# Optimization experiments

Measured on AMD Instinct MI355X. Metric: run time of the kernel, lower is better.

The kernel has to match this reference:

```python
import jax, jax.numpy as jnp
import numpy as np

N_NODES = 100000
N_EDGES = 1600000
DIM_IN, DIM_H, DIM_OUT = 128, 128, 64


def setup_inputs() -> dict:
    key = jax.random.key(0)
    ks = jax.random.split(key, 8)
    s = 0.05
    return {
        "x": jax.random.normal(ks[0], (N_NODES, DIM_IN), jnp.float32),
        "edge_index": jax.random.randint(ks[1], (2, N_EDGES), 0, N_NODES, jnp.int64),
        "W_l1": jax.random.normal(ks[2], (DIM_IN, DIM_H), jnp.float32) * s,
        "W_r1": jax.random.normal(ks[3], (DIM_IN, DIM_H), jnp.float32) * s,
        "b1": jax.random.normal(ks[4], (DIM_H,), jnp.float32) * s,
        "W_l2": jax.random.normal(ks[5], (DIM_H, DIM_OUT), jnp.float32) * s,
        "W_r2": jax.random.normal(ks[6], (DIM_H, DIM_OUT), jnp.float32) * s,
        "b2": jax.random.normal(ks[7], (DIM_OUT,), jnp.float32) * s,
    }


def _sage_conv(h, src, dst, n_nodes, W_l, W_r, b):
    # mean-aggregate neighbor features: gather x[src], scatter-sum to dst, divide by in-degree
    msg = h[src]                                              # [E, d]
    agg = jax.ops.segment_sum(msg, dst, num_segments=n_nodes)  # [N, d]
    deg = jax.ops.segment_sum(jnp.ones((src.shape[0],), h.dtype), dst, num_segments=n_nodes)
    mean = agg / jnp.maximum(deg, 1.0)[:, None]
    # out = lin_l(mean) + lin_r(x) ; bias lives on lin_l (PyG SAGEConv default)
    return mean @ W_l + h @ W_r + b


def reference(x, edge_index, W_l1, W_r1, b1, W_l2, W_r2, b2):
    src, dst = edge_index[0], edge_index[1]
    n = x.shape[0]
    h = jax.nn.relu(_sage_conv(x, src, dst, n, W_l1, W_r1, b1))
    # dropout(p=0.5) is identity in eval mode
    return _sage_conv(h, src, dst, n, W_l2, W_r2, b2)
```

## Files before the change

kernel.cpp:

```cpp
#include <hip/hip_runtime.h>

#define NN 100000
#define NE 1600000

typedef __attribute__((ext_vector_type(8))) short bf16x8;
typedef __attribute__((ext_vector_type(4))) float f32x4;

__device__ __forceinline__ float bf2f(unsigned short b) {
    union { unsigned int u; float f; } v;
    v.u = ((unsigned int)b) << 16;
    return v.f;
}
__device__ __forceinline__ unsigned short f2bf(float f) {
    union { float f; unsigned int u; } v; v.f = f;
    unsigned int u = v.u;
    return (unsigned short)((u + 0x7FFFu + ((u >> 16) & 1u)) >> 16);
}

__global__ void detect_kernel(const int* __restrict__ e, int* __restrict__ flag) {
    int t = blockIdx.x * blockDim.x + threadIdx.x;
    if (t < 4096 && e[2 * t + 1] != 0) atomicOr(flag, 1);
}

__device__ __forceinline__ int esrc(const int* e, int mode, int i) {
    return mode ? e[i] : e[2 * i];
}
__device__ __forceinline__ int edst(const int* e, int mode, int i) {
    return mode ? e[NE + i] : e[2 * (NE + i)];
}

#define NRANGE 4
#define RSZ 25000
#define NCHUNK 64
#define EPC (NE / NCHUNK)
#define GS 100352

__global__ __launch_bounds__(1024) void histA_kernel(
    const int* __restrict__ e, const int* __restrict__ flag, int* __restrict__ G) {
    __shared__ int lh[RSZ];
    const int bid = blockIdx.x;
    const int r = bid & (NRANGE - 1);
    const int c = bid >> 2;
    const int lo = r * RSZ;
    for (int idx = threadIdx.x; idx < RSZ; idx += 1024) lh[idx] = 0;
    __syncthreads();
    const int mode = *flag;
    const int base = c * EPC;
    for (int i = base + threadIdx.x; i < base + EPC; i += 1024) {
        int dl = edst(e, mode, i) - lo;
        if ((unsigned)dl < (unsigned)RSZ) atomicAdd(&lh[dl], 1);
    }
    __syncthreads();
    for (int idx = threadIdx.x; idx < RSZ; idx += 1024)
        G[(size_t)c * GS + lo + idx] = lh[idx];
}

__global__ __launch_bounds__(1024) void scatterC_kernel(
    const int* __restrict__ e, const int* __restrict__ flag,
    const int* __restrict__ S, const int* __restrict__ G, int* __restrict__ csr) {
    __shared__ int sOff[RSZ];
    const int bid = blockIdx.x;
    const int r = bid & (NRANGE - 1);
    const int c = bid >> 2;
    const int lo = r * RSZ;
    for (int idx = threadIdx.x; idx < RSZ; idx += 1024)
        sOff[idx] = S[lo + idx] + G[(size_t)c * GS + lo + idx];
    __syncthreads();
    const int mode = *flag;
    const int base = c * EPC;
    for (int i = base + threadIdx.x; i < base + EPC; i += 1024) {
        int dl = edst(e, mode, i) - lo;
        if ((unsigned)dl < (unsigned)RSZ) {
            int s = esrc(e, mode, i);
            csr[atomicAdd(&sOff[dl], 1)] = s;
        }
    }
}

#define PREF_B 391
#define CVT_G 6250

__global__ __launch_bounds__(256) void prefix_cvt_kernel(
    int* __restrict__ G, int* __restrict__ S,
    const float* __restrict__ xin, unsigned short* __restrict__ xb) {
    if (blockIdx.x < PREF_B) {
        int d = blockIdx.x * 256 + threadIdx.x;
        if (d >= NN) return;
        int run = 0;
#pragma unroll 8
        for (int c = 0; c < NCHUNK; c++) {
            size_t idx = (size_t)c * GS + d;
            int t = G[idx];
            G[idx] = run;
            run += t;
        }
        S[d] = run;
    } else {
        long long i = ((long long)(blockIdx.x - PREF_B) * 256 + threadIdx.x) * 8;
        float4 a = *(const float4*)(xin + i);
        float4 b = *(const float4*)(xin + i + 4);
        bf16x8 rv;
        rv[0] = (short)f2bf(a.x); rv[1] = (short)f2bf(a.y);
        rv[2] = (short)f2bf(a.z); rv[3] = (short)f2bf(a.w);
        rv[4] = (short)f2bf(b.x); rv[5] = (short)f2bf(b.y);
        rv[6] = (short)f2bf(b.z); rv[7] = (short)f2bf(b.w);
        *(bf16x8*)(xb + i) = rv;
    }
}

#define SCAN_G 392

__global__ __launch_bounds__(256) void blocksum_kernel(const int* __restrict__ S,
                                                       int* __restrict__ part) {
    int i = blockIdx.x * 256 + threadIdx.x;
    int v = (i < NN) ? S[i] : 0;
#pragma unroll
    for (int off = 32; off; off >>= 1) v += __shfl_down(v, off, 64);
    __shared__ int wsum[4];
    if ((threadIdx.x & 63) == 0) wsum[threadIdx.x >> 6] = v;
    __syncthreads();
    if (threadIdx.x == 0)
        part[blockIdx.x] = wsum[0] + wsum[1] + wsum[2] + wsum[3];
}

__global__ __launch_bounds__(512) void partscan_kernel(int* __restrict__ part) {
    __shared__ int lds[512];
    const int t = threadIdx.x;
    int v = (t < SCAN_G) ? part[t] : 0;
    lds[t] = v;
    __syncthreads();
    for (int off = 1; off < 512; off <<= 1) {
        int u = (t >= off) ? lds[t - off] : 0;
        __syncthreads();
        lds[t] += u;
        __syncthreads();
    }
    if (t < SCAN_G) part[t] = lds[t] - v;
}

__global__ __launch_bounds__(256) void scanfin_kernel(int* __restrict__ S,
                                                      const int* __restrict__ part) {
    __shared__ int lds[256];
    const int t = threadIdx.x;
    const int i = blockIdx.x * 256 + t;
    int v = (i < NN) ? S[i] : 0;
    lds[t] = v;
    __syncthreads();
    for (int off = 1; off < 256; off <<= 1) {
        int u = (t >= off) ? lds[t - off] : 0;
        __syncthreads();
        lds[t] += u;
        __syncthreads();
    }
    if (i < NN) S[i] = lds[t] - v + part[blockIdx.x];
}

template <int D>
__global__ __launch_bounds__(256) void gather_mean_bf16(
    const unsigned short* __restrict__ feat, const int* __restrict__ csr,
    const int* __restrict__ S, unsigned short* __restrict__ out) {
    constexpr int TPN = D / 8;
    constexpr int NPB = 256 / TPN;
    const int tid = threadIdx.x;
    const int node = blockIdx.x * NPB + tid / TPN;
    const int c = tid % TPN;
    if (node >= NN) return;
    const int begin = S[node];
    const int end = (node == NN - 1) ? NE : S[node + 1];
    float acc0[8] = {0.f, 0.f, 0.f, 0.f, 0.f, 0.f, 0.f, 0.f};
    float acc1[8] = {0.f, 0.f, 0.f, 0.f, 0.f, 0.f, 0.f, 0.f};
    int j = begin;
    for (; j + 8 <= end; j += 8) {
        int s0 = csr[j], s1 = csr[j + 1], s2 = csr[j + 2], s3 = csr[j + 3];
        int s4 = csr[j + 4], s5 = csr[j + 5], s6 = csr[j + 6], s7 = csr[j + 7];
        bf16x8 v0 = *(const bf16x8*)(feat + (size_t)s0 * D + 8 * c);
        bf16x8 v1 = *(const bf16x8*)(feat + (size_t)s1 * D + 8 * c);
        bf16x8 v2 = *(const bf16x8*)(feat + (size_t)s2 * D + 8 * c);
        bf16x8 v3 = *(const bf16x8*)(feat + (size_t)s3 * D + 8 * c);
        bf16x8 v4 = *(const bf16x8*)(feat + (size_t)s4 * D + 8 * c);
        bf16x8 v5 = *(const bf16x8*)(feat + (size_t)s5 * D + 8 * c);
        bf16x8 v6 = *(const bf16x8*)(feat + (size_t)s6 * D + 8 * c);
        bf16x8 v7 = *(const bf16x8*)(feat + (size_t)s7 * D + 8 * c);
#pragma unroll
        for (int q = 0; q < 8; q++) {
            acc0[q] += (bf2f((unsigned short)v0[q]) + bf2f((unsigned short)v2[q])) +
                       (bf2f((unsigned short)v4[q]) + bf2f((unsigned short)v6[q]));
            acc1[q] += (bf2f((unsigned short)v1[q]) + bf2f((unsigned short)v3[q])) +
                       (bf2f((unsigned short)v5[q]) + bf2f((unsigned short)v7[q]));
        }
    }
    for (; j + 2 <= end; j += 2) {
        int s0 = csr[j], s1 = csr[j + 1];
        bf16x8 v0 = *(const bf16x8*)(feat + (size_t)s0 * D + 8 * c);
        bf16x8 v1 = *(const bf16x8*)(feat + (size_t)s1 * D + 8 * c);
#pragma unroll
        for (int q = 0; q < 8; q++) {
            acc0[q] += bf2f((unsigned short)v0[q]);
            acc1[q] += bf2f((unsigned short)v1[q]);
        }
    }
    if (j < end) {
        int s = csr[j];
        bf16x8 v = *(const bf16x8*)(feat + (size_t)s * D + 8 * c);
#pragma unroll
        for (int q = 0; q < 8; q++) acc0[q] += bf2f((unsigned short)v[q]);
    }
    const float inv = 1.0f / fmaxf((float)(end - begin), 1.0f);
    bf16x8 r;
#pragma unroll
    for (int q = 0; q < 8; q++) r[q] = (short)f2bf((acc0[q] + acc1[q]) * inv);
    *(bf16x8*)(out + (size_t)node * D + 8 * c) = r;
}

template <int NO, bool DUAL, bool EADD, bool RELU, bool BIAS, bool OUTF32>
__global__ __launch_bounds__(256, 2) void mfma_gemm(
    const unsigned short* __restrict__ A,
    const unsigned short* __restrict__ X,
    const float* __restrict__ Wa,
    const float* __restrict__ Wb,
    const float* __restrict__ bias,
    const unsigned short* __restrict__ E,
    void* __restrict__ Yv, int N) {
    constexpr int NT = NO / 16;
    constexpr int PITCH = 136;
    __shared__ unsigned short sWb[NO * PITCH];
    __shared__ unsigned short sWa[DUAL ? NO * PITCH : 8];

    const int tid = threadIdx.x;
    for (int idx = tid; idx < 128 * NO; idx += 256) {
        int k = idx / NO, n = idx % NO;
        sWb[n * PITCH + k] = f2bf(Wb[idx]);
        if constexpr (DUAL) sWa[n * PITCH + k] = f2bf(Wa[idx]);
    }
    __syncthreads();

    const int lane = tid & 63;
    const int wv = tid >> 6;
    const int r16 = lane & 15;
    const int kg = lane >> 4;
    const long long rowbase = (long long)blockIdx.x * 128 + wv * 32;

    bf16x8 xf[2][4], af[2][4];
    const bf16x8 zz = {0, 0, 0, 0, 0, 0, 0, 0};
#pragma unroll
    for (int rt = 0; rt < 2; rt++) {
        long long row = rowbase + rt * 16 + r16;
        bool ok = row < N;
#pragma unroll
        for (int ks = 0; ks < 4; ks++) {
            xf[rt][ks] = ok ? *(const bf16x8*)(X + row * 128 + ks * 32 + kg * 8) : zz;
            if constexpr (DUAL)
                af[rt][ks] = ok ? *(const bf16x8*)(A + row * 128 + ks * 32 + kg * 8) : zz;
        }
    }

    f32x4 acc[2][NT];
#pragma unroll
    for (int t = 0; t < NT; t++) {
        float bv = 0.f;
        if constexpr (BIAS) bv = bias[t * 16 + r16];
#pragma unroll
        for (int rt = 0; rt < 2; rt++) acc[rt][t] = (f32x4){bv, bv, bv, bv};
    }

#pragma unroll
    for (int t = 0; t < NT; t++) {
        const unsigned short* wp = &sWb[(t * 16 + r16) * PITCH + kg * 8];
        bf16x8 bb[4];
#pragma unroll
        for (int ks = 0; ks < 4; ks++) bb[ks] = *(const bf16x8*)(wp + ks * 32);
        bf16x8 ba[4];
        if constexpr (DUAL) {
            const unsigned short* wq = &sWa[(t * 16 + r16) * PITCH + kg * 8];
#pragma unroll
            for (int ks = 0; ks < 4; ks++) ba[ks] = *(const bf16x8*)(wq + ks * 32);
        }
#pragma unroll
        for (int rt = 0; rt < 2; rt++) {
#pragma unroll
            for (int ks = 0; ks < 4; ks++) {
                acc[rt][t] = __builtin_amdgcn_mfma_f32_16x16x32_bf16(
                    xf[rt][ks], bb[ks], acc[rt][t], 0, 0, 0);
                if constexpr (DUAL)
                    acc[rt][t] = __builtin_amdgcn_mfma_f32_16x16x32_bf16(
                        af[rt][ks], ba[ks], acc[rt][t], 0, 0, 0);
            }
        }
    }

#pragma unroll
    for (int rt = 0; rt < 2; rt++) {
#pragma unroll
        for (int r = 0; r < 4; r++) {
            long long row = rowbase + rt * 16 + kg * 4 + r;
            if (row < N) {
#pragma unroll
                for (int t = 0; t < NT; t++) {
                    int col = t * 16 + r16;
                    float v = acc[rt][t][r];
                    if constexpr (EADD) v += bf2f(E[row * NO + col]);
                    if constexpr (RELU) v = fmaxf(v, 0.f);
                    if constexpr (OUTF32) ((float*)Yv)[row * NO + col] = v;
                    else ((unsigned short*)Yv)[row * NO + col] = f2bf(v);
                }
            }
        }
    }
}

extern "C" void kernel_launch(void* const* d_in, const int* in_sizes, int n_in,
                              void* d_out, int out_size, void* d_ws, size_t ws_size,
                              hipStream_t stream) {
    const float* x    = (const float*)d_in[0];
    const int*   e32  = (const int*)d_in[1];
    const float* W_l1 = (const float*)d_in[2];
    const float* W_r1 = (const float*)d_in[3];
    const float* b1   = (const float*)d_in[4];
    const float* W_l2 = (const float*)d_in[5];
    const float* W_r2 = (const float*)d_in[6];
    const float* b2   = (const float*)d_in[7];
    float* out = (float*)d_out;

    int* wsI = (int*)d_ws;
    int* flag = wsI;
    int* S    = wsI + 1024;
    int* part = wsI + 1024 + 100352;
    int* csr  = wsI + 101888;
    unsigned short* xb = (unsigned short*)(wsI + 1701888);
    int* G = wsI + 8101888;
    unsigned short* mean1b = (unsigned short*)(wsI + 8101888);
    unsigned short* hb     = (unsigned short*)(wsI + 14524416);
    unsigned short* t2b    = xb;
    unsigned short* mean2b = xb + (size_t)NN * 64;

    hipMemsetAsync(d_ws, 0, 4096, stream);

    detect_kernel<<<16, 256, 0, stream>>>(e32, flag);
    histA_kernel<<<NRANGE * NCHUNK, 1024, 0, stream>>>(e32, flag, G);
    prefix_cvt_kernel<<<PREF_B + CVT_G, 256, 0, stream>>>(G, S, x, xb);
    blocksum_kernel<<<SCAN_G, 256, 0, stream>>>(S, part);
    partscan_kernel<<<1, 512, 0, stream>>>(part);
    scanfin_kernel<<<SCAN_G, 256, 0, stream>>>(S, part);
    scatterC_kernel<<<NRANGE * NCHUNK, 1024, 0, stream>>>(e32, flag, S, G, csr);

    gather_mean_bf16<128><<<6250, 256, 0, stream>>>(xb, csr, S, mean1b);

    mfma_gemm<128, true, false, true, true, false>
        <<<782, 256, 0, stream>>>(mean1b, xb, W_l1, W_r1, b1, nullptr, hb, NN);

    mfma_gemm<64, false, false, false, false, false>
        <<<782, 256, 0, stream>>>(nullptr, hb, nullptr, W_l2, nullptr, nullptr, t2b, NN);

    gather_mean_bf16<64><<<3125, 256, 0, stream>>>(t2b, csr, S, mean2b);

    mfma_gemm<64, false, true, false, true, true>
        <<<782, 256, 0, stream>>>(nullptr, hb, nullptr, W_r2, b2, mean2b, out, NN);
}
```

Before: 221.6 us.

## Fuse layer-1 GEMM with both layer-2 projections and fold residual into second gather

Merges the three GEMM kernels into one: after computing h = relu(mean@W_l1 + x@W_r1 + b1) in registers, it stages h through LDS and immediately computes h@W_l2 and h@W_r2 + b2, so the hidden activations are never written to or reread from global memory. The second gather now adds the W_r2 projection and writes the fp32 output directly, which removes one kernel launch and one pass over the data. The gather unroll drops from 8 to 4 edges per step. The cost is extra LDS reloading of weights and larger register pressure in the fused GEMM.

```diff
diff --git a/kernel.cpp b/kernel.cpp
--- a/kernel.cpp
+++ b/kernel.cpp
@@ -155,53 +155,33 @@
     if (i < NN) S[i] = lds[t] - v + part[blockIdx.x];
 }
 
-template <int D>
-__global__ __launch_bounds__(256) void gather_mean_bf16(
+__global__ __launch_bounds__(256) void gather_mean128(
     const unsigned short* __restrict__ feat, const int* __restrict__ csr,
     const int* __restrict__ S, unsigned short* __restrict__ out) {
-    constexpr int TPN = D / 8;
-    constexpr int NPB = 256 / TPN;
     const int tid = threadIdx.x;
-    const int node = blockIdx.x * NPB + tid / TPN;
-    const int c = tid % TPN;
+    const int node = blockIdx.x * 16 + (tid >> 4);
+    const int c = tid & 15;
     if (node >= NN) return;
     const int begin = S[node];
     const int end = (node == NN - 1) ? NE : S[node + 1];
     float acc0[8] = {0.f, 0.f, 0.f, 0.f, 0.f, 0.f, 0.f, 0.f};
     float acc1[8] = {0.f, 0.f, 0.f, 0.f, 0.f, 0.f, 0.f, 0.f};
     int j = begin;
-    for (; j + 8 <= end; j += 8) {
+    for (; j + 4 <= end; j += 4) {
         int s0 = csr[j], s1 = csr[j + 1], s2 = csr[j + 2], s3 = csr[j + 3];
-        int s4 = csr[j + 4], s5 = csr[j + 5], s6 = csr[j + 6], s7 = csr[j + 7];
-        bf16x8 v0 = *(const bf16x8*)(feat + (size_t)s0 * D + 8 * c);
-        bf16x8 v1 = *(const bf16x8*)(feat + (size_t)s1 * D + 8 * c);
-        bf16x8 v2 = *(const bf16x8*)(feat + (size_t)s2 * D + 8 * c);
-        bf16x8 v3 = *(const bf16x8*)(feat + (size_t)s3 * D + 8 * c);
-        bf16x8 v4 = *(const bf16x8*)(feat + (size_t)s4 * D + 8 * c);
-        bf16x8 v5 = *(const bf16x8*)(feat + (size_t)s5 * D + 8 * c);
-        bf16x8 v6 = *(const bf16x8*)(feat + (size_t)s6 * D + 8 * c);
-        bf16x8 v7 = *(const bf16x8*)(feat + (size_t)s7 * D + 8 * c);
+        bf16x8 v0 = *(const bf16x8*)(feat + (size_t)s0 * 128 + 8 * c);
+        bf16x8 v1 = *(const bf16x8*)(feat + (size_t)s1 * 128 + 8 * c);
+        bf16x8 v2 = *(const bf16x8*)(feat + (size_t)s2 * 128 + 8 * c);
+        bf16x8 v3 = *(const bf16x8*)(feat + (size_t)s3 * 128 + 8 * c);
 #pragma unroll
         for (int q = 0; q < 8; q++) {
-            acc0[q] += (bf2f((unsigned short)v0[q]) + bf2f((unsigned short)v2[q])) +
-                       (bf2f((unsigned short)v4[q]) + bf2f((unsigned short)v6[q]));
-            acc1[q] += (bf2f((unsigned short)v1[q]) + bf2f((unsigned short)v3[q])) +
-                       (bf2f((unsigned short)v5[q]) + bf2f((unsigned short)v7[q]));
-        }
-    }
-    for (; j + 2 <= end; j += 2) {
-        int s0 = csr[j], s1 = csr[j + 1];
-        bf16x8 v0 = *(const bf16x8*)(feat + (size_t)s0 * D + 8 * c);
-        bf16x8 v1 = *(const bf16x8*)(feat + (size_t)s1 * D + 8 * c);
-#pragma unroll
-        for (int q = 0; q < 8; q++) {
-            acc0[q] += bf2f((unsigned short)v0[q]);
-            acc1[q] += bf2f((unsigned short)v1[q]);
-        }
-    }
-    if (j < end) {
+            acc0[q] += bf2f((unsigned short)v0[q]) + bf2f((unsigned short)v2[q]);
+            acc1[q] += bf2f((unsigned short)v1[q]) + bf2f((unsigned short)v3[q]);
+        }
+    }
+    for (; j < end; j++) {
         int s = csr[j];
-        bf16x8 v = *(const bf16x8*)(feat + (size_t)s * D + 8 * c);
+        bf16x8 v = *(const bf16x8*)(feat + (size_t)s * 128 + 8 * c);
 #pragma unroll
         for (int q = 0; q < 8; q++) acc0[q] += bf2f((unsigned short)v[q]);
     }
@@ -209,28 +189,26 @@
     bf16x8 r;
 #pragma unroll
     for (int q = 0; q < 8; q++) r[q] = (short)f2bf((acc0[q] + acc1[q]) * inv);
-    *(bf16x8*)(out + (size_t)node * D + 8 * c) = r;
-}
-
-template <int NO, bool DUAL, bool EADD, bool RELU, bool BIAS, bool OUTF32>
-__global__ __launch_bounds__(256, 2) void mfma_gemm(
+    *(bf16x8*)(out + (size_t)node * 128 + 8 * c) = r;
+}
+
+__global__ __launch_bounds__(256, 2) void mega_gemm(
     const unsigned short* __restrict__ A,
     const unsigned short* __restrict__ X,
-    const float* __restrict__ Wa,
-    const float* __restrict__ Wb,
-    const float* __restrict__ bias,
-    const unsigned short* __restrict__ E,
-    void* __restrict__ Yv, int N) {
-    constexpr int NT = NO / 16;
+    const float* __restrict__ W_l1, const float* __restrict__ W_r1,
+    const float* __restrict__ b1,
+    const float* __restrict__ W_l2, const float* __restrict__ W_r2,
+    const float* __restrict__ b2,
+    unsigned short* __restrict__ T2, unsigned short* __restrict__ P3, int N) {
     constexpr int PITCH = 136;
-    __shared__ unsigned short sWb[NO * PITCH];
-    __shared__ unsigned short sWa[DUAL ? NO * PITCH : 8];
+    __shared__ unsigned short sWb[128 * PITCH];
+    __shared__ unsigned short sWa[128 * PITCH];
 
     const int tid = threadIdx.x;
-    for (int idx = tid; idx < 128 * NO; idx += 256) {
-        int k = idx / NO, n = idx % NO;
-        sWb[n * PITCH + k] = f2bf(Wb[idx]);
-        if constexpr (DUAL) sWa[n * PITCH + k] = f2bf(Wa[idx]);
+    for (int idx = tid; idx < 128 * 128; idx += 256) {
+        int k = idx >> 7, n = idx & 127;
+        sWa[n * PITCH + k] = f2bf(W_l1[idx]);
+        sWb[n * PITCH + k] = f2bf(W_r1[idx]);
     }
     __syncthreads();
 
@@ -249,31 +227,27 @@
 #pragma unroll
         for (int ks = 0; ks < 4; ks++) {
             xf[rt][ks] = ok ? *(const bf16x8*)(X + row * 128 + ks * 32 + kg * 8) : zz;
-            if constexpr (DUAL)
-                af[rt][ks] = ok ? *(const bf16x8*)(A + row * 128 + ks * 32 + kg * 8) : zz;
-        }
-    }
-
-    f32x4 acc[2][NT];
-#pragma unroll
-    for (int t = 0; t < NT; t++) {
-        float bv = 0.f;
-        if constexpr (BIAS) bv = bias[t * 16 + r16];
+            af[rt][ks] = ok ? *(const bf16x8*)(A + row * 128 + ks * 32 + kg * 8) : zz;
+        }
+    }
+
+    f32x4 acc[2][8];
+#pragma unroll
+    for (int t = 0; t < 8; t++) {
+        float bv = b1[t * 16 + r16];
 #pragma unroll
         for (int rt = 0; rt < 2; rt++) acc[rt][t] = (f32x4){bv, bv, bv, bv};
     }
 
 #pragma unroll
-    for (int t = 0; t < NT; t++) {
+    for (int t = 0; t < 8; t++) {
         const unsigned short* wp = &sWb[(t * 16 + r16) * PITCH + kg * 8];
-        bf16x8 bb[4];
-#pragma unroll
-        for (int ks = 0; ks < 4; ks++) bb[ks] = *(const bf16x8*)(wp + ks * 32);
-        bf16x8 ba[4];
-        if constexpr (DUAL) {
-            const unsigned short* wq = &sWa[(t * 16 + r16) * PITCH + kg * 8];
-#pragma unroll
-            for (int ks = 0; ks < 4; ks++) ba[ks] = *(const bf16x8*)(wq + ks * 32);
+        const unsigned short* wq = &sWa[(t * 16 + r16) * PITCH + kg * 8];
+        bf16x8 bb[4], ba[4];
+#pragma unroll
+        for (int ks = 0; ks < 4; ks++) {
+            bb[ks] = *(const bf16x8*)(wp + ks * 32);
+            ba[ks] = *(const bf16x8*)(wq + ks * 32);
         }
 #pragma unroll
         for (int rt = 0; rt < 2; rt++) {
@@ -281,31 +255,141 @@
             for (int ks = 0; ks < 4; ks++) {
                 acc[rt][t] = __builtin_amdgcn_mfma_f32_16x16x32_bf16(
                     xf[rt][ks], bb[ks], acc[rt][t], 0, 0, 0);
-                if constexpr (DUAL)
-                    acc[rt][t] = __builtin_amdgcn_mfma_f32_16x16x32_bf16(
-                        af[rt][ks], ba[ks], acc[rt][t], 0, 0, 0);
+                acc[rt][t] = __builtin_amdgcn_mfma_f32_16x16x32_bf16(
+                    af[rt][ks], ba[ks], acc[rt][t], 0, 0, 0);
             }
         }
     }
 
-#pragma unroll
-    for (int rt = 0; rt < 2; rt++) {
-#pragma unroll
-        for (int r = 0; r < 4; r++) {
-            long long row = rowbase + rt * 16 + kg * 4 + r;
-            if (row < N) {
-#pragma unroll
-                for (int t = 0; t < NT; t++) {
-                    int col = t * 16 + r16;
-                    float v = acc[rt][t][r];
-                    if constexpr (EADD) v += bf2f(E[row * NO + col]);
-                    if constexpr (RELU) v = fmaxf(v, 0.f);
-                    if constexpr (OUTF32) ((float*)Yv)[row * NO + col] = v;
-                    else ((unsigned short*)Yv)[row * NO + col] = f2bf(v);
-                }
+    __syncthreads();
+
+    for (int idx = tid; idx < 128 * 64; idx += 256) {
+        int k = idx >> 6, n = idx & 63;
+        sWa[n * PITCH + k] = f2bf(W_l2[idx]);
+        sWa[64 * PITCH + n * PITCH + k] = f2bf(W_r2[idx]);
+    }
+    unsigned short* sh = sWb + wv * 32 * PITCH;
+#pragma unroll
+    for (int rt = 0; rt < 2; rt++)
+#pragma unroll
+        for (int t = 0; t < 8; t++)
+#pragma unroll
+            for (int r = 0; r < 4; r++)
+                sh[(rt * 16 + kg * 4 + r) * PITCH + t * 16 + r16] =
+                    f2bf(fmaxf(acc[rt][t][r], 0.f));
+    __syncthreads();
+
+    bf16x8 hf[2][4];
+#pragma unroll
+    for (int rt = 0; rt < 2; rt++)
+#pragma unroll
+        for (int ks = 0; ks < 4; ks++)
+            hf[rt][ks] = *(const bf16x8*)(sh + (rt * 16 + r16) * PITCH + ks * 32 + kg * 8);
+
+    {
+        f32x4 o[2][4];
+#pragma unroll
+        for (int t = 0; t < 4; t++)
+#pragma unroll
+            for (int rt = 0; rt < 2; rt++) o[rt][t] = (f32x4){0.f, 0.f, 0.f, 0.f};
+#pragma unroll
+        for (int t = 0; t < 4; t++) {
+            const unsigned short* wp = &sWa[(t * 16 + r16) * PITCH + kg * 8];
+            bf16x8 bb[4];
+#pragma unroll
+            for (int ks = 0; ks < 4; ks++) bb[ks] = *(const bf16x8*)(wp + ks * 32);
+#pragma unroll
+            for (int rt = 0; rt < 2; rt++)
+#pragma unroll
+                for (int ks = 0; ks < 4; ks++)
+                    o[rt][t] = __builtin_amdgcn_mfma_f32_16x16x32_bf16(
+                        hf[rt][ks], bb[ks], o[rt][t], 0, 0, 0);
+        }
+#pragma unroll
+        for (int rt = 0; rt < 2; rt++)
+#pragma unroll
+            for (int r = 0; r < 4; r++) {
+                long long row = rowbase + rt * 16 + kg * 4 + r;
+                if (row < N)
+#pragma unroll
+                    for (int t = 0; t < 4; t++)
+                        T2[row * 64 + t * 16 + r16] = f2bf(o[rt][t][r]);
             }
-        }
-    }
+    }
+    {
+        f32x4 o[2][4];
+#pragma unroll
+        for (int t = 0; t < 4; t++) {
+            float bv = b2[t * 16 + r16];
+#pragma unroll
+            for (int rt = 0; rt < 2; rt++) o[rt][t] = (f32x4){bv, bv, bv, bv};
+        }
+#pragma unroll
+        for (int t = 0; t < 4; t++) {
+            const unsigned short* wp = &sWa[64 * PITCH + (t * 16 + r16) * PITCH + kg * 8];
+            bf16x8 bb[4];
+#pragma unroll
+            for (int ks = 0; ks < 4; ks++) bb[ks] = *(const bf16x8*)(wp + ks * 32);
+#pragma unroll
+            for (int rt = 0; rt < 2; rt++)
+#pragma unroll
+                for (int ks = 0; ks < 4; ks++)
+                    o[rt][t] = __builtin_amdgcn_mfma_f32_16x16x32_bf16(
+                        hf[rt][ks], bb[ks], o[rt][t], 0, 0, 0);
+        }
+#pragma unroll
+        for (int rt = 0; rt < 2; rt++)
+#pragma unroll
+            for (int r = 0; r < 4; r++) {
+                long long row = rowbase + rt * 16 + kg * 4 + r;
+                if (row < N)
+#pragma unroll
+                    for (int t = 0; t < 4; t++)
+                        P3[row * 64 + t * 16 + r16] = f2bf(o[rt][t][r]);
+            }
+    }
+}
+
+__global__ __launch_bounds__(256) void gather2_fused(
+    const unsigned short* __restrict__ t2, const unsigned short* __restrict__ p3,
+    const int* __restrict__ csr, const int* __restrict__ S, float* __restrict__ out) {
+    const int tid = threadIdx.x;
+    const int node = blockIdx.x * 32 + (tid >> 3);
+    const int c = tid & 7;
+    if (node >= NN) return;
+    const int begin = S[node];
+    const int end = (node == NN - 1) ? NE : S[node + 1];
+    float acc0[8] = {0.f, 0.f, 0.f, 0.f, 0.f, 0.f, 0.f, 0.f};
+    float acc1[8] = {0.f, 0.f, 0.f, 0.f, 0.f, 0.f, 0.f, 0.f};
+    int j = begin;
+    for (; j + 4 <= end; j += 4) {
+        int s0 = csr[j], s1 = csr[j + 1], s2 = csr[j + 2], s3 = csr[j + 3];
+        bf16x8 v0 = *(const bf16x8*)(t2 + (size_t)s0 * 64 + 8 * c);
+        bf16x8 v1 = *(const bf16x8*)(t2 + (size_t)s1 * 64 + 8 * c);
+        bf16x8 v2 = *(const bf16x8*)(t2 + (size_t)s2 * 64 + 8 * c);
+        bf16x8 v3 = *(const bf16x8*)(t2 + (size_t)s3 * 64 + 8 * c);
+#pragma unroll
+        for (int q = 0; q < 8; q++) {
+            acc0[q] += bf2f((unsigned short)v0[q]) + bf2f((unsigned short)v2[q]);
+            acc1[q] += bf2f((unsigned short)v1[q]) + bf2f((unsigned short)v3[q]);
+        }
+    }
+    for (; j < end; j++) {
+        int s = csr[j];
+        bf16x8 v = *(const bf16x8*)(t2 + (size_t)s * 64 + 8 * c);
+#pragma unroll
+        for (int q = 0; q < 8; q++) acc0[q] += bf2f((unsigned short)v[q]);
+    }
+    const float inv = 1.0f / fmaxf((float)(end - begin), 1.0f);
+    bf16x8 pv = *(const bf16x8*)(p3 + (size_t)node * 64 + 8 * c);
+    f32x4 r0, r1;
+#pragma unroll
+    for (int q = 0; q < 4; q++) {
+        r0[q] = (acc0[q] + acc1[q]) * inv + bf2f((unsigned short)pv[q]);
+        r1[q] = (acc0[4 + q] + acc1[4 + q]) * inv + bf2f((unsigned short)pv[4 + q]);
+    }
+    *(f32x4*)(out + (size_t)node * 64 + 8 * c) = r0;
+    *(f32x4*)(out + (size_t)node * 64 + 8 * c + 4) = r1;
 }
 
 extern "C" void kernel_launch(void* const* d_in, const int* in_sizes, int n_in,
@@ -324,14 +408,13 @@
     int* wsI = (int*)d_ws;
     int* flag = wsI;
     int* S    = wsI + 1024;
-    int* part = wsI + 1024 + 100352;
+    int* part = wsI + 101376;
     int* csr  = wsI + 101888;
     unsigned short* xb = (unsigned short*)(wsI + 1701888);
     int* G = wsI + 8101888;
     unsigned short* mean1b = (unsigned short*)(wsI + 8101888);
-    unsigned short* hb     = (unsigned short*)(wsI + 14524416);
-    unsigned short* t2b    = xb;
-    unsigned short* mean2b = xb + (size_t)NN * 64;
+    unsigned short* t2b    = (unsigned short*)(wsI + 14524416);
+    unsigned short* p3b    = (unsigned short*)(wsI + 17724416);
 
     hipMemsetAsync(d_ws, 0, 4096, stream);
 
@@ -343,16 +426,10 @@
     scanfin_kernel<<<SCAN_G, 256, 0, stream>>>(S, part);
     scatterC_kernel<<<NRANGE * NCHUNK, 1024, 0, stream>>>(e32, flag, S, G, csr);
 
-    gather_mean_bf16<128><<<6250, 256, 0, stream>>>(xb, csr, S, mean1b);
-
-    mfma_gemm<128, true, false, true, true, false>
-        <<<782, 256, 0, stream>>>(mean1b, xb, W_l1, W_r1, b1, nullptr, hb, NN);
-
-    mfma_gemm<64, false, false, false, false, false>
-        <<<782, 256, 0, stream>>>(nullptr, hb, nullptr, W_l2, nullptr, nullptr, t2b, NN);
-
-    gather_mean_bf16<64><<<3125, 256, 0, stream>>>(t2b, csr, S, mean2b);
-
-    mfma_gemm<64, false, true, false, true, true>
-        <<<782, 256, 0, stream>>>(nullptr, hb, nullptr, W_r2, b2, mean2b, out, NN);
-}
+    gather_mean128<<<6250, 256, 0, stream>>>(xb, csr, S, mean1b);
+
+    mega_gemm<<<782, 256, 0, stream>>>(mean1b, xb, W_l1, W_r1, b1,
+                                       W_l2, W_r2, b2, t2b, p3b, NN);
+
+    gather2_fused<<<3125, 256, 0, stream>>>(t2b, p3b, csr, S, out);
+}
```

Measured after the change: 206.4 us. -6.9%, faster.
